# Optimization experiments

Hardware: AMD Instinct MI355X
Metric: run time of the kernel (lower is better)

Reference implementation:

```python
import jax, jax.numpy as jnp
import numpy as np

N_NODES = 10000
N_EDGES = 320000
F_IN = 128


def _mlp2(h, W1, b1, W2, b2):
    h = jax.nn.relu(h @ W1 + b1)
    return jax.nn.relu(h @ W2 + b2)


def edge_conv(x, src, dst, W1, b1, W2, b2, num_nodes):
    # DGCNN-style EdgeConv: per-edge message MLP(concat(x_i, x_j - x_i)), max-agg per node i
    xi = x[dst]                      # [E, F] center node features
    xj = x[src]                      # [E, F] neighbor features
    m = jnp.concatenate([xi, xj - xi], axis=-1)  # [E, 2F]
    h = _mlp2(m, W1, b1, W2, b2)     # [E, F_out]
    agg = jax.ops.segment_max(h, dst, num_segments=num_nodes)  # [N, F_out]
    # nodes with no incoming edges get -inf from segment_max; zero them
    return jnp.where(jnp.isfinite(agg), agg, 0.0)


def setup_inputs() -> dict:
    key = jax.random.key(0)
    ks = jax.random.split(key, 16)
    s = 0.05
    x = jax.random.normal(ks[0], (N_NODES, F_IN), dtype=jnp.float32)
    edge_index = jax.random.randint(ks[1], (2, N_EDGES), 0, N_NODES)
    # EdgeConvE 1: MLP(512, 256), input 2*128=256
    W1a = jax.random.normal(ks[2], (2 * F_IN, 512), dtype=jnp.float32) * s
    b1a = jnp.zeros((512,), dtype=jnp.float32)
    W2a = jax.random.normal(ks[3], (512, 256), dtype=jnp.float32) * s
    b2a = jnp.zeros((256,), dtype=jnp.float32)
    # EdgeConvE 2: MLP(256, 128), input 2*256=512
    W1b = jax.random.normal(ks[4], (512, 256), dtype=jnp.float32) * s
    b1b = jnp.zeros((256,), dtype=jnp.float32)
    W2b = jax.random.normal(ks[5], (256, 128), dtype=jnp.float32) * s
    b2b = jnp.zeros((128,), dtype=jnp.float32)
    # Dense head
    W3 = jax.random.normal(ks[6], (128, 64), dtype=jnp.float32) * s
    b3 = jnp.zeros((64,), dtype=jnp.float32)
    W4 = jax.random.normal(ks[7], (64, 1), dtype=jnp.float32) * s
    b4 = jnp.zeros((1,), dtype=jnp.float32)
    return {"x": x, "edge_index": edge_index,
            "W1a": W1a, "b1a": b1a, "W2a": W2a, "b2a": b2a,
            "W1b": W1b, "b1b": b1b, "W2b": W2b, "b2b": b2b,
            "W3": W3, "b3": b3, "W4": W4, "b4": b4}


def reference(x, edge_index, W1a, b1a, W2a, b2a, W1b, b1b, W2b, b2b, W3, b3, W4, b4):
    src, dst = edge_index[0], edge_index[1]
    h = edge_conv(x, src, dst, W1a, b1a, W2a, b2a, N_NODES)   # [N, 256]
    h = edge_conv(h, src, dst, W1b, b1b, W2b, b2b, N_NODES)   # [N, 128]
    h = jax.nn.relu(h @ W3 + b3)                               # [N, 64]
    return jax.nn.sigmoid(h @ W4 + b4)                         # [N, 1]
```

## Files before the change

### kernel.cpp

```cpp
#include <hip/hip_runtime.h>
#include <hip/hip_bf16.h>
#include <math.h>

#define NN 10000
#define NE 320000

typedef __attribute__((ext_vector_type(8))) short s8v;
typedef __attribute__((ext_vector_type(4))) float f4v;

__device__ __forceinline__ short f2bf(float f) {
  unsigned u = __float_as_uint(f);
  u = u + 0x7fffu + ((u >> 16) & 1u);
  return (short)(u >> 16);
}
__device__ __forceinline__ float bf2f(short u) {
  return __uint_as_float(((unsigned)(unsigned short)u) << 16);
}
__device__ __forceinline__ unsigned cvt_pair(unsigned wa, unsigned wb) {
  float a0 = __uint_as_float(wa << 16);
  float a1 = __uint_as_float(wa & 0xFFFF0000u);
  float b0 = __uint_as_float(wb << 16);
  float b1 = __uint_as_float(wb & 0xFFFF0000u);
  float s0 = fmaxf(a0 + b0, 0.f);
  float s1 = fmaxf(a1 + b1, 0.f);
  __hip_bfloat162 h = __float22bfloat162_rn(float2{s0, s1});
  unsigned u; __builtin_memcpy(&u, &h, 4);
  return u;
}

__global__ void hist_kernel(const int* __restrict__ ei, int* __restrict__ cnt) {
  int e = blockIdx.x * 256 + threadIdx.x;
  if (e < NE) atomicAdd(&cnt[ei[NE + e]], 1);
}

__global__ void __launch_bounds__(1024)
scan_kernel(const int* __restrict__ cnt, int* __restrict__ cur) {
  __shared__ int part[1024];
  const int t = threadIdx.x;
  const int base = t * 10;
  int local[10];
  int s = 0;
#pragma unroll
  for (int u = 0; u < 10; ++u) {
    int c = (base + u < NN) ? cnt[base + u] : 0;
    local[u] = s; s += c;
  }
  part[t] = s;
  __syncthreads();
  for (int off = 1; off < 1024; off <<= 1) {
    int v = part[t];
    int w = (t >= off) ? part[t - off] : 0;
    __syncthreads();
    part[t] = v + w;
    __syncthreads();
  }
  int excl = (t == 0) ? 0 : part[t - 1];
#pragma unroll
  for (int u = 0; u < 10; ++u)
    if (base + u < NN) cur[base + u] = excl + local[u];
}

__global__ void scatter_kernel(const int* __restrict__ ei, int* __restrict__ cur,
                               int* __restrict__ sSrc, int* __restrict__ sDst) {
  int e = blockIdx.x * 256 + threadIdx.x;
  if (e < NE) {
    int d = ei[NE + e];
    int p = atomicAdd(&cur[d], 1);
    sSrc[p] = ei[e];
    sDst[p] = d;
  }
}

__global__ void prep_weights(const float* __restrict__ W1a, const float* __restrict__ W1b,
                             const float* __restrict__ W2a, const float* __restrict__ W2b,
                             short* __restrict__ Wp1T, short* __restrict__ Wp2T,
                             short* __restrict__ BTf1, short* __restrict__ BTf2) {
  int i = blockIdx.x * 256 + threadIdx.x;
  if (i < 131072) {
    int j = i >> 7, k = i & 127;
    float v;
    if (j < 512) v = W1a[k * 512 + j] - W1a[(k + 128) * 512 + j];
    else         v = W1a[(k + 128) * 512 + (j - 512)];
    Wp1T[i] = f2bf(v);
  } else if (i < 262144) {
    int t = i - 131072;
    int j = t >> 8, k = t & 255;
    float v;
    if (j < 256) v = W1b[k * 256 + j] - W1b[(k + 256) * 256 + j];
    else         v = W1b[(k + 256) * 256 + (j - 256)];
    Wp2T[t] = f2bf(v);
  } else if (i < 393216) {
    int t = i - 262144;
    int n = t >> 9, k = t & 511;
    BTf1[(k >> 5) * 8192 + n * 32 + (k & 31)] = f2bf(W2a[k * 256 + n]);
  } else if (i < 425984) {
    int t = i - 393216;
    int n = t >> 8, k = t & 255;
    BTf2[(k >> 5) * 4096 + n * 32 + (k & 31)] = f2bf(W2b[k * 128 + n]);
  }
}

template<int K>
__global__ void __launch_bounds__(256)
node_gemm(const float* __restrict__ A, const short* __restrict__ BT,
          const float* __restrict__ bias, int biasLen,
          short* __restrict__ C, int Ntot) {
  const int rowBase = blockIdx.x * 64;
  const int wave = threadIdx.x >> 6, lane = threadIdx.x & 63;
  const int colBase = blockIdx.y * 256 + wave * 64;
  const int lm = lane & 15, q = lane >> 4;
  f4v acc[4][4] = {};
  int arow[4];
#pragma unroll
  for (int mt = 0; mt < 4; ++mt) {
    int r = rowBase + mt * 16 + lm;
    arow[mt] = r < NN ? r : NN - 1;
  }
  for (int kk = 0; kk < K; kk += 32) {
    const int k = kk + q * 8;
    s8v aF[4], bF[4];
#pragma unroll
    for (int mt = 0; mt < 4; ++mt) {
      const float4* ap = (const float4*)(A + (size_t)arow[mt] * K + k);
      float4 x0 = ap[0], x1 = ap[1];
      s8v t;
      t[0] = f2bf(x0.x); t[1] = f2bf(x0.y); t[2] = f2bf(x0.z); t[3] = f2bf(x0.w);
      t[4] = f2bf(x1.x); t[5] = f2bf(x1.y); t[6] = f2bf(x1.z); t[7] = f2bf(x1.w);
      aF[mt] = t;
    }
#pragma unroll
    for (int nt = 0; nt < 4; ++nt)
      bF[nt] = *(const s8v*)(BT + (size_t)(colBase + nt * 16 + lm) * K + k);
#pragma unroll
    for (int mt = 0; mt < 4; ++mt)
#pragma unroll
      for (int nt = 0; nt < 4; ++nt)
        acc[mt][nt] = __builtin_amdgcn_mfma_f32_16x16x32_bf16(aF[mt], bF[nt], acc[mt][nt], 0, 0, 0);
  }
#pragma unroll
  for (int nt = 0; nt < 4; ++nt) {
    int col = colBase + nt * 16 + lm;
    float bv = (col < biasLen) ? bias[col] : 0.0f;
#pragma unroll
    for (int mt = 0; mt < 4; ++mt) {
#pragma unroll
      for (int i = 0; i < 4; ++i) {
        int row = rowBase + mt * 16 + q * 4 + i;
        if (row < NN) C[(size_t)row * Ntot + col] = f2bf(acc[mt][nt][i] + bv);
      }
    }
  }
}

template<int K, int NT>
__global__ void __launch_bounds__(256, 4)
edge_gemm_pf(const short* __restrict__ AB, const short* __restrict__ BTf,
             const float* __restrict__ bias,
             const int* __restrict__ sSrc, const int* __restrict__ sDst,
             int* __restrict__ y) {
  constexpr int KT = 64;
  constexpr int KTP = 72;
  constexpr int TILES = K / KT;
  constexpr int NW = NT / 4;
  constexpr int NTL = NW / 16;
  __shared__ __align__(16) short hA[2][64 * KTP];
  __shared__ int srcS[64], dstS[64];
  __shared__ int segSt[65];
  __shared__ int segDst[64];
  __shared__ int segAtm[64];
  __shared__ __align__(4) unsigned char rowSidC[64];
  __shared__ int segD;

  const int tid = threadIdx.x;
  const int eBase = blockIdx.x * 64;
  const int wave = tid >> 6, lane = tid & 63, lm = lane & 15, q = lane >> 4;
  const int cBase = wave * NW;

  if (tid < 64) { srcS[tid] = sSrc[eBase + tid]; dstS[tid] = sDst[eBase + tid]; }
  __syncthreads();

  if (tid < 64) {
    int d = dstS[tid];
    int prev = (tid == 0) ? -1 : dstS[tid - 1];
    bool flag = (d != prev);
    unsigned long long mask = __ballot(flag);
    int Dtot = __popcll(mask);
    int sid = __popcll(mask & (0xFFFFFFFFFFFFFFFFull >> (63 - tid))) - 1;
    rowSidC[tid] = (unsigned char)sid;
    if (tid == 0) { segD = Dtot; segSt[Dtot] = 64; }
    if (flag) {
      int idx = sid;
      segSt[idx] = tid;
      segDst[idx] = d;
      bool atm = false;
      if (idx == 0 && eBase > 0 && sDst[eBase - 1] == d) atm = true;
      if (idx == Dtot - 1 && eBase + 64 < NE && sDst[eBase + 64] == d) atm = true;
      segAtm[idx] = atm ? 1 : 0;
    }
  }

  const int r0 = tid >> 3, kc0 = (tid & 7) * 8;
  const int r1 = r0 + 32;
  const size_t dO0 = (size_t)dstS[r0] * (2 * K) + kc0;
  const size_t sO0 = (size_t)srcS[r0] * (2 * K) + K + kc0;
  const size_t dO1 = (size_t)dstS[r1] * (2 * K) + kc0;
  const size_t sO1 = (size_t)srcS[r1] * (2 * K) + K + kc0;

  f4v acc[4][NTL] = {};

  uint4 av0 = *(const uint4*)(AB + dO0);
  uint4 bv0 = *(const uint4*)(AB + sO0);
  uint4 av1 = *(const uint4*)(AB + dO1);
  uint4 bv1 = *(const uint4*)(AB + sO1);

  for (int t = 0; t < TILES; ++t) {
    s8v bF0[NTL];
#pragma unroll
    for (int nt = 0; nt < NTL; ++nt)
      bF0[nt] = *(const s8v*)(BTf + (size_t)(t * 2) * (NT * 32) +
                              (cBase + nt * 16 + lm) * 32 + q * 8);
    short* hbuf = hA[t & 1];
    {
      uint4 o;
      o.x = cvt_pair(av0.x, bv0.x); o.y = cvt_pair(av0.y, bv0.y);
      o.z = cvt_pair(av0.z, bv0.z); o.w = cvt_pair(av0.w, bv0.w);
      *(uint4*)(&hbuf[r0 * KTP + kc0]) = o;
      uint4 o1;
      o1.x = cvt_pair(av1.x, bv1.x); o1.y = cvt_pair(av1.y, bv1.y);
      o1.z = cvt_pair(av1.z, bv1.z); o1.w = cvt_pair(av1.w, bv1.w);
      *(uint4*)(&hbuf[r1 * KTP + kc0]) = o1;
    }
    if (t + 1 < TILES) {
      const int kn = (t + 1) * KT;
      av0 = *(const uint4*)(AB + dO0 + kn);
      bv0 = *(const uint4*)(AB + sO0 + kn);
      av1 = *(const uint4*)(AB + dO1 + kn);
      bv1 = *(const uint4*)(AB + sO1 + kn);
    }
    __syncthreads();
    {
      const int kl = q * 8;
#pragma unroll
      for (int mt = 0; mt < 4; ++mt) {
        s8v aF = *(const s8v*)(&hbuf[(mt * 16 + lm) * KTP + kl]);
#pragma unroll
        for (int nt = 0; nt < NTL; ++nt)
          acc[mt][nt] = __builtin_amdgcn_mfma_f32_16x16x32_bf16(aF, bF0[nt], acc[mt][nt], 0, 0, 0);
      }
    }
    {
      s8v bF1[NTL];
#pragma unroll
      for (int nt = 0; nt < NTL; ++nt)
        bF1[nt] = *(const s8v*)(BTf + (size_t)(t * 2 + 1) * (NT * 32) +
                                (cBase + nt * 16 + lm) * 32 + q * 8);
      const int kl = 32 + q * 8;
#pragma unroll
      for (int mt = 0; mt < 4; ++mt) {
        s8v aF = *(const s8v*)(&hbuf[(mt * 16 + lm) * KTP + kl]);
#pragma unroll
        for (int nt = 0; nt < NTL; ++nt)
          acc[mt][nt] = __builtin_amdgcn_mfma_f32_16x16x32_bf16(aF, bF1[nt], acc[mt][nt], 0, 0, 0);
      }
    }
  }

  const int D = segD;
  int sid[4][4];
#pragma unroll
  for (int mt = 0; mt < 4; ++mt) {
    unsigned pk = *(const unsigned*)(&rowSidC[mt * 16 + q * 4]);
#pragma unroll
    for (int i = 0; i < 4; ++i) sid[mt][i] = (int)((pk >> (8 * i)) & 255u);
  }
#pragma unroll
  for (int nt = 0; nt < NTL; ++nt) {
    const int col = cBase + nt * 16 + lm;
    const float bvv = bias[col];
    for (int s = 0; s < D; ++s) {
      float m = -1e30f;
#pragma unroll
      for (int mt = 0; mt < 4; ++mt)
#pragma unroll
        for (int i = 0; i < 4; ++i)
          m = fmaxf(m, sid[mt][i] == s ? acc[mt][nt][i] : -1e30f);
      m = fmaxf(m, __shfl_xor(m, 16));
      m = fmaxf(m, __shfl_xor(m, 32));
      if (q == 0) {
        float v = m + bvv;
        int* addr = &y[(size_t)segDst[s] * NT + col];
        if (segAtm[s]) {
          if (v > 0.f) atomicMax(addr, __float_as_int(v));
        } else {
          *addr = __float_as_int(fmaxf(v, 0.f));
        }
      }
    }
  }
}

__global__ void __launch_bounds__(64)
head_kernel(const float* __restrict__ y2, const float* __restrict__ W3,
            const float* __restrict__ b3, const float* __restrict__ W4,
            const float* __restrict__ b4, float* __restrict__ out) {
  const int n = blockIdx.x, j = threadIdx.x;
  const float* yr = y2 + (size_t)n * 128;
  float acc = 0.f;
#pragma unroll
  for (int k = 0; k < 128; ++k) acc += yr[k] * W3[k * 64 + j];
  acc += b3[j];
  float h = acc > 0.f ? acc : 0.f;
  float p = h * W4[j];
#pragma unroll
  for (int off = 32; off; off >>= 1) p += __shfl_down(p, off);
  if (j == 0) {
    float z = p + b4[0];
    out[n] = 1.f / (1.f + expf(-z));
  }
}

__global__ void diag_kernel(float* out, float v) { out[0] = v; }

extern "C" void kernel_launch(void* const* d_in, const int* in_sizes, int n_in,
                              void* d_out, int out_size, void* d_ws, size_t ws_size,
                              hipStream_t stream) {
  const float* x   = (const float*)d_in[0];
  const int*   ei  = (const int*)d_in[1];
  const float* W1a = (const float*)d_in[2];
  const float* b1a = (const float*)d_in[3];
  const float* W2a = (const float*)d_in[4];
  const float* b2a = (const float*)d_in[5];
  const float* W1b = (const float*)d_in[6];
  const float* b1b = (const float*)d_in[7];
  const float* W2b = (const float*)d_in[8];
  const float* b2b = (const float*)d_in[9];
  const float* W3  = (const float*)d_in[10];
  const float* b3  = (const float*)d_in[11];
  const float* W4  = (const float*)d_in[12];
  const float* b4  = (const float*)d_in[13];

  char* ws = (char*)d_ws;
  short* Wp1T = (short*)(ws + 0);
  short* Wp2T = (short*)(ws + 262144);
  short* BTf1 = (short*)(ws + 524288);
  short* BTf2 = (short*)(ws + 786432);
  short* A1B1 = (short*)(ws + 851968);
  short* A2B2 = (short*)(ws + 851968);
  int*   Y1   = (int*)(ws + 21331968);
  int*   Y2   = (int*)(ws + 21331968);
  int*   cnt  = (int*)(ws + 31571968);
  int*   cur  = (int*)(ws + 31611968);
  int*   sSrc = (int*)(ws + 31651968);
  int*   sDst = (int*)(ws + 32931968);

  if (ws_size < 34211968) {
    diag_kernel<<<1, 1, 0, stream>>>((float*)d_out, (float)ws_size);
    return;
  }

  hipMemsetAsync(cnt, 0, 40000, stream);
  hist_kernel<<<1250, 256, 0, stream>>>(ei, cnt);
  scan_kernel<<<1, 1024, 0, stream>>>(cnt, cur);
  scatter_kernel<<<1250, 256, 0, stream>>>(ei, cur, sSrc, sDst);

  prep_weights<<<1664, 256, 0, stream>>>(W1a, W1b, W2a, W2b, Wp1T, Wp2T, BTf1, BTf2);

  node_gemm<128><<<dim3(157, 4), 256, 0, stream>>>(x, Wp1T, b1a, 512, A1B1, 1024);
  hipMemsetAsync(Y1, 0, (size_t)NN * 256 * 4, stream);
  edge_gemm_pf<512, 256><<<5000, 256, 0, stream>>>(A1B1, BTf1, b2a, sSrc, sDst, Y1);

  node_gemm<256><<<dim3(157, 2), 256, 0, stream>>>((const float*)Y1, Wp2T, b1b, 256, A2B2, 512);
  hipMemsetAsync(Y2, 0, (size_t)NN * 128 * 4, stream);
  edge_gemm_pf<256, 128><<<5000, 256, 0, stream>>>(A2B2, BTf2, b2b, sSrc, sDst, Y2);

  head_kernel<<<NN, 64, 0, stream>>>((const float*)Y2, W3, b3, W4, b4, (float*)d_out);
}
```

Before: 408.5 us.

## Process 128 edges per block with 8 waves sharing weight fragments

Doubles the edge tile per block to 128 rows with 512 threads: two row groups of four waves each share the same column slice of the second-layer weights, so each weight fragment loaded from global memory serves twice as many edges. Segment-boundary metadata is now computed per 64-row half, and the atomic flags look at the neighbouring half or the neighbouring block. It also raises wave priority around the MFMA sections with s_setprio. The trade-offs are more LDS per block, fewer blocks, and a 512-thread launch bound that may limit registers per thread.

```diff
diff --git a/kernel.cpp b/kernel.cpp
--- a/kernel.cpp
+++ b/kernel.cpp
@@ -153,65 +153,72 @@
 }
 
 template<int K, int NT>
-__global__ void __launch_bounds__(256, 4)
+__global__ void __launch_bounds__(512, 4)
 edge_gemm_pf(const short* __restrict__ AB, const short* __restrict__ BTf,
              const float* __restrict__ bias,
              const int* __restrict__ sSrc, const int* __restrict__ sDst,
              int* __restrict__ y) {
+  constexpr int ROWS = 128;
   constexpr int KT = 64;
   constexpr int KTP = 72;
   constexpr int TILES = K / KT;
-  constexpr int NW = NT / 4;
-  constexpr int NTL = NW / 16;
-  __shared__ __align__(16) short hA[2][64 * KTP];
-  __shared__ int srcS[64], dstS[64];
-  __shared__ int segSt[65];
-  __shared__ int segDst[64];
-  __shared__ int segAtm[64];
-  __shared__ __align__(4) unsigned char rowSidC[64];
-  __shared__ int segD;
+  constexpr int WCOLS = NT / 4;
+  constexpr int NTL = WCOLS / 16;
+  __shared__ __align__(16) short hA[2][ROWS * KTP];
+  __shared__ int srcS[ROWS], dstS[ROWS];
+  __shared__ int segDst[2][64];
+  __shared__ int segAtm[2][64];
+  __shared__ __align__(4) unsigned char rowSidC[ROWS];
+  __shared__ int segD[2];
 
   const int tid = threadIdx.x;
-  const int eBase = blockIdx.x * 64;
+  const int eBase = blockIdx.x * ROWS;
   const int wave = tid >> 6, lane = tid & 63, lm = lane & 15, q = lane >> 4;
-  const int cBase = wave * NW;
-
-  if (tid < 64) { srcS[tid] = sSrc[eBase + tid]; dstS[tid] = sDst[eBase + tid]; }
+  const int cg = wave & 3, rg = wave >> 2;
+  const int cBase = cg * WCOLS;
+  const int rg64 = rg * 64;
+
+  if (tid < ROWS) { srcS[tid] = sSrc[eBase + tid]; dstS[tid] = sDst[eBase + tid]; }
   __syncthreads();
 
-  if (tid < 64) {
-    int d = dstS[tid];
-    int prev = (tid == 0) ? -1 : dstS[tid - 1];
-    bool flag = (d != prev);
-    unsigned long long mask = __ballot(flag);
-    int Dtot = __popcll(mask);
-    int sid = __popcll(mask & (0xFFFFFFFFFFFFFFFFull >> (63 - tid))) - 1;
-    rowSidC[tid] = (unsigned char)sid;
-    if (tid == 0) { segD = Dtot; segSt[Dtot] = 64; }
-    if (flag) {
-      int idx = sid;
-      segSt[idx] = tid;
-      segDst[idx] = d;
-      bool atm = false;
-      if (idx == 0 && eBase > 0 && sDst[eBase - 1] == d) atm = true;
-      if (idx == Dtot - 1 && eBase + 64 < NE && sDst[eBase + 64] == d) atm = true;
-      segAtm[idx] = atm ? 1 : 0;
-    }
-  }
-
   const int r0 = tid >> 3, kc0 = (tid & 7) * 8;
-  const int r1 = r0 + 32;
+  const int r1 = r0 + 64;
   const size_t dO0 = (size_t)dstS[r0] * (2 * K) + kc0;
   const size_t sO0 = (size_t)srcS[r0] * (2 * K) + K + kc0;
   const size_t dO1 = (size_t)dstS[r1] * (2 * K) + kc0;
   const size_t sO1 = (size_t)srcS[r1] * (2 * K) + K + kc0;
 
-  f4v acc[4][NTL] = {};
-
   uint4 av0 = *(const uint4*)(AB + dO0);
   uint4 bv0 = *(const uint4*)(AB + sO0);
   uint4 av1 = *(const uint4*)(AB + dO1);
   uint4 bv1 = *(const uint4*)(AB + sO1);
+
+  if (tid < 2 * 64) {
+    const int w = tid >> 6;
+    const int r = tid & 63;
+    const int row = tid;
+    int d = dstS[row];
+    int prev = (r == 0) ? -1 : dstS[row - 1];
+    bool flag = (r == 0) || (d != prev);
+    unsigned long long mask = __ballot(flag);
+    int Dtot = __popcll(mask);
+    int sid = __popcll(mask & (0xFFFFFFFFFFFFFFFFull >> (63 - r))) - 1;
+    rowSidC[row] = (unsigned char)sid;
+    if (r == 0) segD[w] = Dtot;
+    if (flag) {
+      int prevOut = (w == 1) ? dstS[63]
+                             : ((eBase > 0) ? sDst[eBase - 1] : -1);
+      int nextOut = (w == 0) ? dstS[64]
+                             : ((eBase + ROWS < NE) ? sDst[eBase + ROWS] : -1);
+      bool atm = false;
+      if (sid == 0 && prevOut == d) atm = true;
+      if (sid == Dtot - 1 && nextOut == d) atm = true;
+      segDst[w][sid] = d;
+      segAtm[w][sid] = atm ? 1 : 0;
+    }
+  }
+
+  f4v acc[4][NTL] = {};
 
   for (int t = 0; t < TILES; ++t) {
     s8v bF0[NTL];
@@ -240,13 +247,15 @@
     __syncthreads();
     {
       const int kl = q * 8;
+      __builtin_amdgcn_s_setprio(1);
 #pragma unroll
       for (int mt = 0; mt < 4; ++mt) {
-        s8v aF = *(const s8v*)(&hbuf[(mt * 16 + lm) * KTP + kl]);
+        s8v aF = *(const s8v*)(&hbuf[(rg64 + mt * 16 + lm) * KTP + kl]);
 #pragma unroll
         for (int nt = 0; nt < NTL; ++nt)
           acc[mt][nt] = __builtin_amdgcn_mfma_f32_16x16x32_bf16(aF, bF0[nt], acc[mt][nt], 0, 0, 0);
       }
+      __builtin_amdgcn_s_setprio(0);
     }
     {
       s8v bF1[NTL];
@@ -255,21 +264,23 @@
         bF1[nt] = *(const s8v*)(BTf + (size_t)(t * 2 + 1) * (NT * 32) +
                                 (cBase + nt * 16 + lm) * 32 + q * 8);
       const int kl = 32 + q * 8;
+      __builtin_amdgcn_s_setprio(1);
 #pragma unroll
       for (int mt = 0; mt < 4; ++mt) {
-        s8v aF = *(const s8v*)(&hbuf[(mt * 16 + lm) * KTP + kl]);
+        s8v aF = *(const s8v*)(&hbuf[(rg64 + mt * 16 + lm) * KTP + kl]);
 #pragma unroll
         for (int nt = 0; nt < NTL; ++nt)
           acc[mt][nt] = __builtin_amdgcn_mfma_f32_16x16x32_bf16(aF, bF1[nt], acc[mt][nt], 0, 0, 0);
       }
-    }
-  }
-
-  const int D = segD;
+      __builtin_amdgcn_s_setprio(0);
+    }
+  }
+
+  const int D = segD[rg];
   int sid[4][4];
 #pragma unroll
   for (int mt = 0; mt < 4; ++mt) {
-    unsigned pk = *(const unsigned*)(&rowSidC[mt * 16 + q * 4]);
+    unsigned pk = *(const unsigned*)(&rowSidC[rg64 + mt * 16 + q * 4]);
 #pragma unroll
     for (int i = 0; i < 4; ++i) sid[mt][i] = (int)((pk >> (8 * i)) & 255u);
   }
@@ -288,8 +299,8 @@
       m = fmaxf(m, __shfl_xor(m, 32));
       if (q == 0) {
         float v = m + bvv;
-        int* addr = &y[(size_t)segDst[s] * NT + col];
-        if (segAtm[s]) {
+        int* addr = &y[(size_t)segDst[rg][s] * NT + col];
+        if (segAtm[rg][s]) {
           if (v > 0.f) atomicMax(addr, __float_as_int(v));
         } else {
           *addr = __float_as_int(fmaxf(v, 0.f));
@@ -367,11 +378,11 @@
 
   node_gemm<128><<<dim3(157, 4), 256, 0, stream>>>(x, Wp1T, b1a, 512, A1B1, 1024);
   hipMemsetAsync(Y1, 0, (size_t)NN * 256 * 4, stream);
-  edge_gemm_pf<512, 256><<<5000, 256, 0, stream>>>(A1B1, BTf1, b2a, sSrc, sDst, Y1);
+  edge_gemm_pf<512, 256><<<2500, 512, 0, stream>>>(A1B1, BTf1, b2a, sSrc, sDst, Y1);
 
   node_gemm<256><<<dim3(157, 2), 256, 0, stream>>>((const float*)Y1, Wp2T, b1b, 256, A2B2, 512);
   hipMemsetAsync(Y2, 0, (size_t)NN * 128 * 4, stream);
-  edge_gemm_pf<256, 128><<<5000, 256, 0, stream>>>(A2B2, BTf2, b2b, sSrc, sDst, Y2);
+  edge_gemm_pf<256, 128><<<2500, 512, 0, stream>>>(A2B2, BTf2, b2b, sSrc, sDst, Y2);
 
   head_kernel<<<NN, 64, 0, stream>>>((const float*)Y2, W3, b3, W4, b4, (float*)d_out);
 }
```

After: 395.5 us. 3.2% less time.
